# Kernel optimization log

Measured on AMD Instinct MI355X. Metric: run time of the kernel, lower is better.

Reference implementation:

```python
import jax, jax.numpy as jnp
import numpy as np

EPS = 5e-06

def setup_inputs() -> dict:
    key = jax.random.key(0)
    k1, k2 = jax.random.split(key)
    B, S, D = 4, 4096, 2048
    input = jax.random.normal(k1, (B, S, D), dtype=jnp.float32)
    gamma = jax.random.uniform(k2, (B, S, D), dtype=jnp.float32)
    return {"input": input, "gamma": gamma}

def reference(input, gamma):
    # RMS over last dim per (i, j): sqrt(mean(x^2) + eps)
    rms = jnp.sqrt(jnp.mean(input * input, axis=-1, keepdims=True) + EPS)
    return input / rms * gamma
```

## Files before the change

kernel.cpp:

```cpp
#include <hip/hip_runtime.h>
#include <hip/hip_bf16.h>


#define D_DIM 2048
#define VEC_PER_ROW (D_DIM / 4)
#define EPS 5e-6f

typedef float f32x4 __attribute__((ext_vector_type(4)));

__global__ __launch_bounds__(256) void rmsnorm_f32_kernel(
    const float4* __restrict__ x,
    const float4* __restrict__ g,
    float4* __restrict__ out)
{
    const int t = threadIdx.x;
    const long base = (long)blockIdx.x * VEC_PER_ROW;

    float4 xv0 = x[base + t];
    float4 xv1 = x[base + t + 256];
    float4 gv0 = g[base + t];
    float4 gv1 = g[base + t + 256];

    float ss = xv0.x * xv0.x + xv0.y * xv0.y + xv0.z * xv0.z + xv0.w * xv0.w
             + xv1.x * xv1.x + xv1.y * xv1.y + xv1.z * xv1.z + xv1.w * xv1.w;

    #pragma unroll
    for (int off = 32; off > 0; off >>= 1)
        ss += __shfl_down(ss, off, 64);

    __shared__ float wsum[4];
    const int wave = t >> 6;
    if ((t & 63) == 0) wsum[wave] = ss;
    __syncthreads();

    const float total = wsum[0] + wsum[1] + wsum[2] + wsum[3];
    const float inv = rsqrtf(total * (1.0f / (float)D_DIM) + EPS);

    float4 o0, o1;
    o0.x = xv0.x * inv * gv0.x;
    o0.y = xv0.y * inv * gv0.y;
    o0.z = xv0.z * inv * gv0.z;
    o0.w = xv0.w * inv * gv0.w;
    o1.x = xv1.x * inv * gv1.x;
    o1.y = xv1.y * inv * gv1.y;
    o1.z = xv1.z * inv * gv1.z;
    o1.w = xv1.w * inv * gv1.w;

    __builtin_nontemporal_store(*(const f32x4*)&o0, (f32x4*)&out[base + t]);
    __builtin_nontemporal_store(*(const f32x4*)&o1, (f32x4*)&out[base + t + 256]);
}

extern "C" void kernel_launch(void* const* d_in, const int* in_sizes, int n_in,
                              void* d_out, int out_size, void* d_ws, size_t ws_size,
                              hipStream_t stream) {
    const float* x = (const float*)d_in[0];
    const float* g = (const float*)d_in[1];
    float* out = (float*)d_out;

    const int rows = out_size / D_DIM;
    rmsnorm_f32_kernel<<<rows, 256, 0, stream>>>(
        (const float4*)x, (const float4*)g, (float4*)out);
}
```

Before: 60.05 us.

## Assign one row per wavefront and drop block-level shared-memory reduction

Each 64-lane wavefront now normalizes a whole row, loading 8 float4 of input and 8 of gamma per lane. The sum of squares is reduced with xor shuffles only, removing the LDS write and __syncthreads. Blocks now cover 4 rows, so the grid shrinks by 4x. More loads in flight per thread raise memory-level parallelism at the cost of higher register use.

```diff
diff --git a/kernel.cpp b/kernel.cpp
--- a/kernel.cpp
+++ b/kernel.cpp
@@ -8,46 +8,45 @@
 
 typedef float f32x4 __attribute__((ext_vector_type(4)));
 
-__global__ __launch_bounds__(256) void rmsnorm_f32_kernel(
+__global__ __launch_bounds__(256) void rmsnorm_wave_kernel(
     const float4* __restrict__ x,
     const float4* __restrict__ g,
     float4* __restrict__ out)
 {
-    const int t = threadIdx.x;
-    const long base = (long)blockIdx.x * VEC_PER_ROW;
+    const int lane = threadIdx.x & 63;
+    const int wv   = threadIdx.x >> 6;
+    const long row = (long)blockIdx.x * 4 + wv;
+    const long base = row * VEC_PER_ROW;
 
-    float4 xv0 = x[base + t];
-    float4 xv1 = x[base + t + 256];
-    float4 gv0 = g[base + t];
-    float4 gv1 = g[base + t + 256];
+    float4 xv[8], gv[8];
+    #pragma unroll
+    for (int k = 0; k < 8; ++k) xv[k] = x[base + lane + 64 * k];
+    #pragma unroll
+    for (int k = 0; k < 8; ++k) gv[k] = g[base + lane + 64 * k];
 
-    float ss = xv0.x * xv0.x + xv0.y * xv0.y + xv0.z * xv0.z + xv0.w * xv0.w
-             + xv1.x * xv1.x + xv1.y * xv1.y + xv1.z * xv1.z + xv1.w * xv1.w;
+    float ss = 0.0f;
+    #pragma unroll
+    for (int k = 0; k < 8; ++k) {
+        ss += xv[k].x * xv[k].x + xv[k].y * xv[k].y
+            + xv[k].z * xv[k].z + xv[k].w * xv[k].w;
+    }
 
     #pragma unroll
     for (int off = 32; off > 0; off >>= 1)
-        ss += __shfl_down(ss, off, 64);
+        ss += __shfl_xor(ss, off, 64);
 
-    __shared__ float wsum[4];
-    const int wave = t >> 6;
-    if ((t & 63) == 0) wsum[wave] = ss;
-    __syncthreads();
+    const float inv = rsqrtf(ss * (1.0f / (float)D_DIM) + EPS);
 
-    const float total = wsum[0] + wsum[1] + wsum[2] + wsum[3];
-    const float inv = rsqrtf(total * (1.0f / (float)D_DIM) + EPS);
-
-    float4 o0, o1;
-    o0.x = xv0.x * inv * gv0.x;
-    o0.y = xv0.y * inv * gv0.y;
-    o0.z = xv0.z * inv * gv0.z;
-    o0.w = xv0.w * inv * gv0.w;
-    o1.x = xv1.x * inv * gv1.x;
-    o1.y = xv1.y * inv * gv1.y;
-    o1.z = xv1.z * inv * gv1.z;
-    o1.w = xv1.w * inv * gv1.w;
-
-    __builtin_nontemporal_store(*(const f32x4*)&o0, (f32x4*)&out[base + t]);
-    __builtin_nontemporal_store(*(const f32x4*)&o1, (f32x4*)&out[base + t + 256]);
+    #pragma unroll
+    for (int k = 0; k < 8; ++k) {
+        float4 o;
+        o.x = xv[k].x * inv * gv[k].x;
+        o.y = xv[k].y * inv * gv[k].y;
+        o.z = xv[k].z * inv * gv[k].z;
+        o.w = xv[k].w * inv * gv[k].w;
+        __builtin_nontemporal_store(*(const f32x4*)&o,
+                                    (f32x4*)&out[base + lane + 64 * k]);
+    }
 }
 
 extern "C" void kernel_launch(void* const* d_in, const int* in_sizes, int n_in,
@@ -58,6 +57,7 @@
     float* out = (float*)d_out;
 
     const int rows = out_size / D_DIM;
-    rmsnorm_f32_kernel<<<rows, 256, 0, stream>>>(
+    const int blocks = rows / 4;
+    rmsnorm_wave_kernel<<<blocks, 256, 0, stream>>>(
         (const float4*)x, (const float4*)g, (float4*)out);
 }
```

After: 61.86 us. 3.0% more time.

## Process eight rows per block with grid-stride loop and next-row prefetch

Applied to the files above, without the earlier changes.

Each block now handles eight rows spaced by the grid stride, with the launch shrunk by the same factor. The next row's x and gamma loads are issued before the current row's reduction, and a sched_barrier keeps them ahead so memory latency overlaps compute. The shared reduction buffer is double-buffered so one barrier per row suffices. This cuts block launch overhead and hides latency, at the cost of higher register use and fewer resident blocks. It also assumes the row count divides evenly by eight.

```diff
diff --git a/kernel.cpp b/kernel.cpp
--- a/kernel.cpp
+++ b/kernel.cpp
@@ -5,49 +5,70 @@
 #define D_DIM 2048
 #define VEC_PER_ROW (D_DIM / 4)
 #define EPS 5e-6f
+#define ROWS_PER_BLOCK 8
 
 typedef float f32x4 __attribute__((ext_vector_type(4)));
 
-__global__ __launch_bounds__(256) void rmsnorm_f32_kernel(
+__global__ __launch_bounds__(256) void rmsnorm_gs_kernel(
     const float4* __restrict__ x,
     const float4* __restrict__ g,
     float4* __restrict__ out)
 {
     const int t = threadIdx.x;
-    const long base = (long)blockIdx.x * VEC_PER_ROW;
+    const int wave = t >> 6;
+    const long stride = gridDim.x;
+
+    long row  = blockIdx.x;
+    long base = row * VEC_PER_ROW;
 
     float4 xv0 = x[base + t];
     float4 xv1 = x[base + t + 256];
     float4 gv0 = g[base + t];
     float4 gv1 = g[base + t + 256];
 
-    float ss = xv0.x * xv0.x + xv0.y * xv0.y + xv0.z * xv0.z + xv0.w * xv0.w
-             + xv1.x * xv1.x + xv1.y * xv1.y + xv1.z * xv1.z + xv1.w * xv1.w;
+    __shared__ float wsum[2][4];
 
     #pragma unroll
-    for (int off = 32; off > 0; off >>= 1)
-        ss += __shfl_down(ss, off, 64);
+    for (int i = 0; i < ROWS_PER_BLOCK; ++i) {
+        const long nbase = base + stride * VEC_PER_ROW;
+        float4 nx0, nx1, ng0, ng1;
+        if (i < ROWS_PER_BLOCK - 1) {
+            nx0 = x[nbase + t];
+            nx1 = x[nbase + t + 256];
+            ng0 = g[nbase + t];
+            ng1 = g[nbase + t + 256];
+        }
+        __builtin_amdgcn_sched_barrier(0);
 
-    __shared__ float wsum[4];
-    const int wave = t >> 6;
-    if ((t & 63) == 0) wsum[wave] = ss;
-    __syncthreads();
+        float ss = xv0.x * xv0.x + xv0.y * xv0.y + xv0.z * xv0.z + xv0.w * xv0.w
+                 + xv1.x * xv1.x + xv1.y * xv1.y + xv1.z * xv1.z + xv1.w * xv1.w;
 
-    const float total = wsum[0] + wsum[1] + wsum[2] + wsum[3];
-    const float inv = rsqrtf(total * (1.0f / (float)D_DIM) + EPS);
+        #pragma unroll
+        for (int off = 32; off > 0; off >>= 1)
+            ss += __shfl_down(ss, off, 64);
 
-    float4 o0, o1;
-    o0.x = xv0.x * inv * gv0.x;
-    o0.y = xv0.y * inv * gv0.y;
-    o0.z = xv0.z * inv * gv0.z;
-    o0.w = xv0.w * inv * gv0.w;
-    o1.x = xv1.x * inv * gv1.x;
-    o1.y = xv1.y * inv * gv1.y;
-    o1.z = xv1.z * inv * gv1.z;
-    o1.w = xv1.w * inv * gv1.w;
+        if ((t & 63) == 0) wsum[i & 1][wave] = ss;
+        __syncthreads();
 
-    __builtin_nontemporal_store(*(const f32x4*)&o0, (f32x4*)&out[base + t]);
-    __builtin_nontemporal_store(*(const f32x4*)&o1, (f32x4*)&out[base + t + 256]);
+        const float total = wsum[i & 1][0] + wsum[i & 1][1]
+                          + wsum[i & 1][2] + wsum[i & 1][3];
+        const float inv = rsqrtf(total * (1.0f / (float)D_DIM) + EPS);
+
+        float4 o0, o1;
+        o0.x = xv0.x * inv * gv0.x;
+        o0.y = xv0.y * inv * gv0.y;
+        o0.z = xv0.z * inv * gv0.z;
+        o0.w = xv0.w * inv * gv0.w;
+        o1.x = xv1.x * inv * gv1.x;
+        o1.y = xv1.y * inv * gv1.y;
+        o1.z = xv1.z * inv * gv1.z;
+        o1.w = xv1.w * inv * gv1.w;
+        __builtin_nontemporal_store(*(const f32x4*)&o0, (f32x4*)&out[base + t]);
+        __builtin_nontemporal_store(*(const f32x4*)&o1, (f32x4*)&out[base + t + 256]);
+
+        xv0 = nx0; xv1 = nx1; gv0 = ng0; gv1 = ng1;
+        base = nbase;
+    }
 }
 
 extern "C" void kernel_launch(void* const* d_in, const int* in_sizes, int n_in,
@@ -58,6 +79,7 @@
     float* out = (float*)d_out;
 
     const int rows = out_size / D_DIM;
-    rmsnorm_f32_kernel<<<rows, 256, 0, stream>>>(
+    const int blocks = rows / ROWS_PER_BLOCK;
+    rmsnorm_gs_kernel<<<blocks, 256, 0, stream>>>(
         (const float4*)x, (const float4*)g, (float4*)out);
 }
```

After: 63.90 us. 1.06x slower.
